# Performance work log

Measured on AMD Instinct MI355X. Metric: run time of the kernel, lower is better.

The kernel has to match this reference:

```python
import jax, jax.numpy as jnp
import numpy as np

NEG_SLOPE = 0.2  # PyG GATConv default negative_slope


def gat_layer(x, src, dst, W, att_src, att_dst, bias, heads, out_ch, n_nodes):
    """PyG-style GATConv (concat=True, add_self_loops already applied via src/dst).
    x: [N, F_in], W: [F_in, heads*out_ch], att_*: [heads, out_ch], bias: [heads*out_ch].
    Returns [N, heads*out_ch]."""
    xh = (x @ W).reshape(n_nodes, heads, out_ch)            # [N,H,C]
    a_src = jnp.einsum('nhc,hc->nh', xh, att_src)           # [N,H]
    a_dst = jnp.einsum('nhc,hc->nh', xh, att_dst)           # [N,H]
    e = a_src[src] + a_dst[dst]                             # [E,H]
    e = jax.nn.leaky_relu(e, NEG_SLOPE)
    # softmax over edges sharing the same destination node
    emax = jax.ops.segment_max(e, dst, num_segments=n_nodes)    # [N,H]
    expe = jnp.exp(e - emax[dst])                           # [E,H]
    denom = jax.ops.segment_sum(expe, dst, num_segments=n_nodes)
    coef = expe / (denom[dst] + 1e-16)                      # [E,H]
    # weighted scatter-aggregate of source features
    msg = xh[src] * coef[:, :, None]                        # [E,H,C]
    out = jax.ops.segment_sum(msg, dst, num_segments=n_nodes)  # [N,H,C]
    return out.reshape(n_nodes, heads * out_ch) + bias


def setup_inputs() -> dict:
    key = jax.random.key(0)
    ks = jax.random.split(key, 10)
    N, E = 50000, 800000
    IN, HID, OUT, H = 4, 60, 96, 8
    x = jax.random.normal(ks[0], (N, IN), dtype=jnp.float32)
    edge_index = jax.random.randint(ks[1], (2, E), 0, N, dtype=jnp.int64)
    s = 0.1
    W1 = jax.random.normal(ks[2], (IN, H * HID), dtype=jnp.float32) * s
    att_src1 = jax.random.normal(ks[3], (H, HID), dtype=jnp.float32) * s
    att_dst1 = jax.random.normal(ks[4], (H, HID), dtype=jnp.float32) * s
    b1 = jnp.zeros((H * HID,), dtype=jnp.float32)
    W2 = jax.random.normal(ks[5], (H * HID, OUT), dtype=jnp.float32) * s
    att_src2 = jax.random.normal(ks[6], (1, OUT), dtype=jnp.float32) * s
    att_dst2 = jax.random.normal(ks[7], (1, OUT), dtype=jnp.float32) * s
    b2 = jnp.zeros((OUT,), dtype=jnp.float32)
    return {"x": x, "edge_index": edge_index,
            "W1": W1, "att_src1": att_src1, "att_dst1": att_dst1, "b1": b1,
            "W2": W2, "att_src2": att_src2, "att_dst2": att_dst2, "b2": b2}


def reference(x, edge_index, W1, att_src1, att_dst1, b1, W2, att_src2, att_dst2, b2):
    N = x.shape[0]
    # add self-loops (PyG GATConv default add_self_loops=True)
    loop = jnp.arange(N, dtype=edge_index.dtype)
    src = jnp.concatenate([edge_index[0], loop])
    dst = jnp.concatenate([edge_index[1], loop])
    # dropout layers are identity in eval mode
    h = gat_layer(x, src, dst, W1, att_src1, att_dst1, b1, heads=8, out_ch=60, n_nodes=N)
    h = jax.nn.elu(h)
    out = gat_layer(h, src, dst, W2, att_src2, att_dst2, b2, heads=1, out_ch=96, n_nodes=N)
    return out
```

## Files before the change

### kernel.cpp

```cpp
#include <hip/hip_runtime.h>
#include <hip/hip_bf16.h>
#include <hip/hip_fp16.h>
#include <cstdint>
#include <cstddef>


typedef _Float16 half8 __attribute__((ext_vector_type(8)));
typedef float floatx4 __attribute__((ext_vector_type(4)));

constexpr int BSH = 7;
constexpr int MAXBUK = 512;

__global__ __launch_bounds__(256) void setup_kernel(
    const float* __restrict__ W1,
    const float* __restrict__ as1, const float* __restrict__ ad1,
    const float* __restrict__ W2,
    const float* __restrict__ as2, const float* __restrict__ ad2,
    const float* __restrict__ x, const int* __restrict__ ei,
    int E, int N,
    float4* __restrict__ w1t, float2* __restrict__ wa2t,
    __half* __restrict__ w2t,
    float* __restrict__ a_s1, float* __restrict__ a_d1,
    int* __restrict__ bcnt,
    int NW2T, int NA1)
{
    __shared__ int   lcnt[MAXBUK];
    __shared__ float wa1s[64];
    int b = blockIdx.x;
    int t = threadIdx.x;
    int A1_0 = 1 + NW2T;
    int H0   = A1_0 + NA1;

    if (b == 0) {
        for (int i = t; i < 480; i += 256) {
            float accs = 0.f, accd = 0.f;
            #pragma unroll 4
            for (int c = 0; c < 96; ++c) {
                float w = W2[i * 96 + c];
                accs += w * as2[c];
                accd += w * ad2[c];
            }
            wa2t[i] = make_float2(accs, accd);
            w1t[i]  = make_float4(W1[i], W1[480 + i], W1[960 + i], W1[1440 + i]);
        }
    } else if (b < A1_0) {
        int idx = (b - 1) * 256 + t;
        if (idx < 96 * 480) {
            int n = idx / 480, k = idx - n * 480;
            w2t[idx] = __float2half(W2[k * 96 + n]);
        }
    } else if (b < H0) {
        if (t < 32) {
            int k = t >> 3, h = t & 7;
            float accs = 0.f, accd = 0.f;
            for (int c = 0; c < 60; ++c) {
                float w = W1[k * 480 + h * 60 + c];
                accs += w * as1[h * 60 + c];
                accd += w * ad1[h * 60 + c];
            }
            wa1s[k * 8 + h]      = accs;
            wa1s[32 + k * 8 + h] = accd;
        }
        __syncthreads();
        int n = (b - A1_0) * 256 + t;
        if (n < N) {
            float4 xv = *(const float4*)(x + (size_t)n * 4);
            #pragma unroll
            for (int h = 0; h < 8; ++h) {
                float as = xv.x * wa1s[h] + xv.y * wa1s[8 + h]
                         + xv.z * wa1s[16 + h] + xv.w * wa1s[24 + h];
                float ad = xv.x * wa1s[32 + h] + xv.y * wa1s[40 + h]
                         + xv.z * wa1s[48 + h] + xv.w * wa1s[56 + h];
                a_s1[n * 8 + h] = as;
                a_d1[n * 8 + h] = ad;
            }
        }
    } else {
        int nbuk = (N + 127) >> BSH;
        for (int i = t; i < nbuk; i += 256) lcnt[i] = 0;
        __syncthreads();
        #pragma unroll
        for (int u = 0; u < 8; ++u) {
            int e = (b - H0) * 2048 + u * 256 + t;
            if (e < E + N) {
                int d = (e < E) ? ei[E + e] : (e - E);
                atomicAdd(&lcnt[d >> BSH], 1);
            }
        }
        __syncthreads();
        for (int i = t; i < nbuk; i += 256)
            if (lcnt[i]) atomicAdd(&bcnt[i], lcnt[i]);
    }
}

__global__ __launch_bounds__(512) void bucket_scan(const int* __restrict__ bcnt, int nbuk,
                                                   int* __restrict__ boff,
                                                   int* __restrict__ bcursor,
                                                   int* __restrict__ row_ptr, int N)
{
    __shared__ int wsum[8];
    int t = threadIdx.x, lane = t & 63, wid = t >> 6;
    int v = (t < nbuk) ? bcnt[t] : 0;
    int x = v;
    #pragma unroll
    for (int off = 1; off < 64; off <<= 1) {
        int y = __shfl_up(x, off, 64);
        if (lane >= off) x += y;
    }
    if (lane == 63) wsum[wid] = x;
    __syncthreads();
    if (wid == 0) {
        int wv = (lane < 8) ? wsum[lane] : 0;
        #pragma unroll
        for (int off = 1; off < 8; off <<= 1) {
            int y = __shfl_up(wv, off, 64);
            if (lane >= off) wv += y;
        }
        if (lane < 8) wsum[lane] = wv;
    }
    __syncthreads();
    int excl = (wid ? wsum[wid - 1] : 0) + x - v;
    if (t < nbuk) { boff[t] = excl; bcursor[t] = excl; }
    if (t == nbuk - 1) { boff[nbuk] = excl + v; row_ptr[N] = excl + v; }
}

__global__ __launch_bounds__(256) void multisplit(const int* __restrict__ ei, int E, int N,
                                                  int* __restrict__ bcursor,
                                                  int2* __restrict__ ebuf)
{
    __shared__ int lcnt[MAXBUK];
    __shared__ int lbase[MAXBUK];
    int t = threadIdx.x;
    int nbuk = (N + 127) >> BSH;
    for (int b = t; b < nbuk; b += 256) lcnt[b] = 0;
    __syncthreads();
    constexpr int U = 16;
    int ss[U], dd[U], rk[U];
    bool ok[U];
    #pragma unroll
    for (int u = 0; u < U; ++u) {
        int e = blockIdx.x * (256 * U) + u * 256 + t;
        ok[u] = e < E + N;
        if (ok[u]) {
            if (e < E) { ss[u] = ei[e]; dd[u] = ei[E + e]; } else { ss[u] = dd[u] = e - E; }
            rk[u] = atomicAdd(&lcnt[dd[u] >> BSH], 1);
        }
    }
    __syncthreads();
    for (int b = t; b < nbuk; b += 256)
        lbase[b] = lcnt[b] ? atomicAdd(&bcursor[b], lcnt[b]) : 0;
    __syncthreads();
    #pragma unroll
    for (int u = 0; u < U; ++u)
        if (ok[u]) ebuf[(size_t)lbase[dd[u] >> BSH] + rk[u]] = make_int2(ss[u], dd[u]);
}

__global__ __launch_bounds__(256) void csrfill2(const int2* __restrict__ ebuf,
                                                const int* __restrict__ boff,
                                                int* __restrict__ row_ptr,
                                                int* __restrict__ csr,
                                                int* __restrict__ csrdst, int N)
{
    int b = blockIdx.x;
    int node0 = b << BSH;
    int nnode = N - node0;  if (nnode > 128) nnode = 128;
    int beg = boff[b], end = boff[b + 1];
    __shared__ int hcnt[128], hcur[128];
    __shared__ int wends[4];
    int t = threadIdx.x;
    if (t < 128) hcnt[t] = 0;
    __syncthreads();
    for (int i = beg + t; i < end; i += 256)
        atomicAdd(&hcnt[ebuf[i].y - node0], 1);
    __syncthreads();
    int lane = t & 63, wid = t >> 6;
    int v = (t < 128) ? hcnt[t] : 0;
    int x = v;
    #pragma unroll
    for (int off = 1; off < 64; off <<= 1) {
        int y = __shfl_up(x, off, 64);
        if (lane >= off) x += y;
    }
    if (lane == 63) wends[wid] = x;
    __syncthreads();
    int excl = x - v + ((wid == 1) ? wends[0] : 0);
    if (t < 128) {
        hcur[t] = excl;
        if (t < nnode) row_ptr[node0 + t] = beg + excl;
    }
    __syncthreads();
    for (int i = beg + t; i < end; i += 256) {
        int2 e = ebuf[i];
        int p = atomicAdd(&hcur[e.y - node0], 1);
        csr[(size_t)beg + p]    = e.x;
        csrdst[(size_t)beg + p] = e.y;
    }
}

__global__ __launch_bounds__(256) void gat1_agg(
    const int* __restrict__ row_ptr, const int* __restrict__ csr,
    const float* __restrict__ x,
    const float* __restrict__ a_s1, const float* __restrict__ a_d1,
    float* __restrict__ agg, float* __restrict__ ssum, int N)
{
    int gid = blockIdx.x * blockDim.x + threadIdx.x;
    int node = gid >> 6;
    if (node >= N) return;
    int lane = threadIdx.x & 63;
    int half = lane >> 5;
    int sl   = lane & 31;
    int h = sl >> 2, c = sl & 3;
    float adh = a_d1[(size_t)node * 8 + h];

    float aggv = 0.f, sv = 0.f;
    int beg = row_ptr[node], end = row_ptr[node + 1];
    constexpr int U = 4;
    for (int base = beg; base < end; base += 2 * U) {
        int   idx[U];
        float msk[U];
        #pragma unroll
        for (int u = 0; u < U; ++u) {
            int t = base + 2 * u + half;
            msk[u] = (t < end) ? 1.f : 0.f;
            idx[u] = csr[t < end ? t : (end - 1)];
        }
        float xv[U], av[U];
        #pragma unroll
        for (int u = 0; u < U; ++u) xv[u] = x[(size_t)idx[u] * 4 + c];
        #pragma unroll
        for (int u = 0; u < U; ++u) av[u] = a_s1[(size_t)idx[u] * 8 + h];
        #pragma unroll
        for (int u = 0; u < U; ++u) {
            float ev = av[u] + adh;
            ev = ev > 0.f ? ev : 0.2f * ev;
            float p = __expf(ev) * msk[u];
            sv   += p;
            aggv += p * xv[u];
        }
    }
    aggv += __shfl_xor(aggv, 32);
    sv   += __shfl_xor(sv, 32);
    if (lane < 32) {
        agg[(size_t)node * 32 + lane] = aggv;
        if (c == 0) ssum[(size_t)node * 8 + h] = sv;
    }
}

__global__ __launch_bounds__(256) void h_kernel(
    const float* __restrict__ agg, const float* __restrict__ ssum,
    const float4* __restrict__ w1t, const float* __restrict__ b1,
    const float2* __restrict__ wa2t,
    __half* __restrict__ h2buf, float* __restrict__ a2s, float* __restrict__ a2d, int N)
{
    __shared__ float4 w1s[480];
    __shared__ float2 wa2s[480];
    __shared__ float  b1s[480];
    int t = threadIdx.x;
    for (int i = t; i < 480; i += 256) {
        w1s[i]  = w1t[i];
        wa2s[i] = wa2t[i];
        b1s[i]  = b1[i];
    }
    __syncthreads();

    int node = blockIdx.x * 4 + (t >> 6);
    if (node >= N) return;
    int lane = t & 63;
    bool act = lane < 60;

    float psrc = 0.f, pdst = 0.f;
    #pragma unroll
    for (int h = 0; h < 8; ++h) {
        float4 ag  = *(const float4*)(agg + (size_t)node * 32 + h * 4);
        float  inv = 1.f / (ssum[(size_t)node * 8 + h] + 1e-16f);
        if (act) {
            int col = h * 60 + lane;
            float4 w  = w1s[col];
            float raw = ag.x * w.x + ag.y * w.y + ag.z * w.z + ag.w * w.w;
            float v   = raw * inv + b1s[col];
            float o   = v > 0.f ? v : (__expf(v) - 1.f);
            h2buf[(size_t)node * 480 + col] = __float2half(o);
            float2 wz = wa2s[col];
            psrc += o * wz.x;
            pdst += o * wz.y;
        }
    }
    #pragma unroll
    for (int off = 32; off; off >>= 1) {
        psrc += __shfl_xor(psrc, off);
        pdst += __shfl_xor(pdst, off);
    }
    if (lane == 0) { a2s[node] = psrc; a2d[node] = pdst; }
}

__global__ __launch_bounds__(256) void p2_kernel(
    const int* __restrict__ csr, const int* __restrict__ csrdst,
    const float* __restrict__ a_s2, const float* __restrict__ a_d2,
    float* __restrict__ pbuf2, int EP)
{
    int i = (blockIdx.x * 256 + threadIdx.x) * 4;
    if (i + 3 < EP) {
        int4 s4 = *(const int4*)(csr + i);
        int4 d4 = *(const int4*)(csrdst + i);
        float e0 = a_s2[s4.x] + a_d2[d4.x];
        float e1 = a_s2[s4.y] + a_d2[d4.y];
        float e2 = a_s2[s4.z] + a_d2[d4.z];
        float e3 = a_s2[s4.w] + a_d2[d4.w];
        float4 o;
        o.x = __expf(fmaxf(e0, 0.2f * e0));
        o.y = __expf(fmaxf(e1, 0.2f * e1));
        o.z = __expf(fmaxf(e2, 0.2f * e2));
        o.w = __expf(fmaxf(e3, 0.2f * e3));
        *(float4*)(pbuf2 + i) = o;
    } else {
        for (int u = 0; u < 4; ++u) {
            int e = i + u;
            if (e < EP) {
                float ev = a_s2[csr[e]] + a_d2[csrdst[e]];
                pbuf2[e] = __expf(fmaxf(ev, 0.2f * ev));
            }
        }
    }
}

__global__ __launch_bounds__(256) void gemm2_mfma(
    const __half* __restrict__ h2, const __half* __restrict__ w2t,
    __half* __restrict__ xh2h, int N)
{
    int wave = threadIdx.x >> 6;
    int lane = threadIdx.x & 63;
    int m0 = blockIdx.x * 64 + wave * 16;
    int ra   = lane & 15;
    int kgrp = lane >> 4;
    int m = m0 + ra;  if (m > N - 1) m = N - 1;

    floatx4 acc[6];
    #pragma unroll
    for (int n = 0; n < 6; ++n) acc[n] = (floatx4){0.f, 0.f, 0.f, 0.f};

    const _Float16* arow = (const _Float16*)(h2 + (size_t)m * 480);
    const _Float16* wt   = (const _Float16*)w2t;
    for (int k0 = 0; k0 < 480; k0 += 32) {
        half8 af = *(const half8*)(arow + k0 + kgrp * 8);
        #pragma unroll
        for (int n = 0; n < 6; ++n) {
            half8 bf = *(const half8*)(wt + (size_t)(n * 16 + ra) * 480 + k0 + kgrp * 8);
            acc[n] = __builtin_amdgcn_mfma_f32_16x16x32_f16(af, bf, acc[n], 0, 0, 0);
        }
    }
    #pragma unroll
    for (int n = 0; n < 6; ++n) {
        int c = n * 16 + ra;
        #pragma unroll
        for (int j = 0; j < 4; ++j) {
            int r = m0 + kgrp * 4 + j;
            if (r < N) xh2h[(size_t)r * 96 + c] = __float2half(acc[n][j]);
        }
    }
}

__global__ __launch_bounds__(256) void gat2_fused(
    const int* __restrict__ row_ptr, const int* __restrict__ csr,
    const float* __restrict__ pbuf2,
    const __half* __restrict__ xh2h, const float* __restrict__ b2,
    float* __restrict__ out, int N)
{
    int gid = blockIdx.x * blockDim.x + threadIdx.x;
    int node = gid >> 6;
    if (node >= N) return;
    int lane = threadIdx.x & 63;
    bool act = lane < 48;
    float s = 0.f, ax = 0.f, ay = 0.f;
    int beg = __builtin_amdgcn_readfirstlane(row_ptr[node]);
    int end = __builtin_amdgcn_readfirstlane(row_ptr[node + 1]);
    constexpr int U = 16;
    for (int e0 = beg; e0 < end; e0 += U) {
        int   srcs[U];
        float pv[U];
        #pragma unroll
        for (int u = 0; u < U; ++u) {
            int t = e0 + u;  if (t > end - 1) t = end - 1;
            srcs[u] = __builtin_amdgcn_readfirstlane(csr[t]);
            float pr = __uint_as_float(
                __builtin_amdgcn_readfirstlane(__float_as_uint(pbuf2[t])));
            pv[u] = (e0 + u < end) ? pr : 0.f;
        }
        __half2 gv[U];
        if (act) {
            #pragma unroll
            for (int u = 0; u < U; ++u)
                gv[u] = ((const __half2*)(xh2h + (size_t)srcs[u] * 96))[lane];
        }
        #pragma unroll
        for (int u = 0; u < U; ++u) {
            s += pv[u];
            if (act) {
                float2 fg = __half22float2(gv[u]);
                ax += pv[u] * fg.x;
                ay += pv[u] * fg.y;
            }
        }
    }
    float inv = 1.f / (s + 1e-16f);
    if (act) {
        out[(size_t)node * 96 + 2 * lane]     = ax * inv + b2[2 * lane];
        out[(size_t)node * 96 + 2 * lane + 1] = ay * inv + b2[2 * lane + 1];
    }
}

extern "C" void kernel_launch(void* const* d_in, const int* in_sizes, int n_in,
                              void* d_out, int out_size, void* d_ws, size_t ws_size,
                              hipStream_t stream)
{
    const float* x   = (const float*)d_in[0];
    const int*   ei  = (const int*)  d_in[1];
    const float* W1  = (const float*)d_in[2];
    const float* as1 = (const float*)d_in[3];
    const float* ad1 = (const float*)d_in[4];
    const float* b1  = (const float*)d_in[5];
    const float* W2  = (const float*)d_in[6];
    const float* as2 = (const float*)d_in[7];
    const float* ad2 = (const float*)d_in[8];
    const float* b2  = (const float*)d_in[9];
    float* out = (float*)d_out;

    int N  = in_sizes[0] / 4;
    int E  = in_sizes[1] / 2;
    int EP = E + N;
    int NBUK  = (N + 127) >> BSH;
    int NW2T  = (96 * 480 + 255) / 256;
    int NA1   = (N + 255) / 256;
    int NBK_H = (EP + 2047) / 2048;
    int NBK_M = (EP + 4095) / 4096;
    int NSETUP = 1 + NW2T + NA1 + NBK_H;

    float* f = (float*)d_ws;
    float* a_s1  = f;  f += (size_t)N * 8;
    float* a_d1  = f;  f += (size_t)N * 8;
    float* agg   = f;  f += (size_t)N * 32;
    float* ssum  = f;  f += (size_t)N * 8;
    float* a_s2  = f;  f += N;
    float* a_d2  = f;  f += N;
    float4* w1t  = (float4*)f;  f += 480 * 4;
    float2* wa2t = (float2*)f;  f += 480 * 2;
    __half* h2buf = (__half*)f;
    __half* hp   = h2buf + (size_t)N * 480;
    __half* xh2h = hp;   hp += (size_t)N * 96;
    __half* w2t  = hp;   hp += 96 * 480;
    int2* ebuf   = (int2*)hp;
    int* ip      = (int*)(ebuf + EP);
    int* row_ptr = ip;  ip += N + 1;
    int* bcnt    = ip;  ip += MAXBUK;
    int* boff    = ip;  ip += MAXBUK + 1;
    int* bcursor = ip;  ip += MAXBUK;
    int* csr     = ip;  ip += EP;
    int* csrdst  = ip;  ip += EP;
    float* pbuf2 = (float*)ip;  ip += EP;

    size_t needed = (size_t)((char*)ip - (char*)d_ws);
    if (needed > ws_size) return;

    hipMemsetAsync(bcnt, 0, MAXBUK * sizeof(int), stream);
    setup_kernel<<<NSETUP, 256, 0, stream>>>(
        W1, as1, ad1, W2, as2, ad2, x, ei, E, N,
        w1t, wa2t, w2t, a_s1, a_d1, bcnt, NW2T, NA1);
    bucket_scan<<<1, 512, 0, stream>>>(bcnt, NBUK, boff, bcursor, row_ptr, N);
    multisplit<<<NBK_M, 256, 0, stream>>>(ei, E, N, bcursor, ebuf);
    csrfill2<<<NBUK, 256, 0, stream>>>(ebuf, boff, row_ptr, csr, csrdst, N);
    gat1_agg<<<(N * 64 + 255) / 256, 256, 0, stream>>>(
        row_ptr, csr, x, a_s1, a_d1, agg, ssum, N);
    h_kernel<<<(N + 3) / 4, 256, 0, stream>>>(
        agg, ssum, w1t, b1, wa2t, h2buf, a_s2, a_d2, N);
    p2_kernel<<<(EP + 1023) / 1024, 256, 0, stream>>>(
        csr, csrdst, a_s2, a_d2, pbuf2, EP);
    gemm2_mfma<<<(N + 63) / 64, 256, 0, stream>>>(h2buf, w2t, xh2h, N);
    gat2_fused<<<(N * 64 + 255) / 256, 256, 0, stream>>>(
        row_ptr, csr, pbuf2, xh2h, b2, out, N);
}
```

Baseline: 191.8 us.

## Fuse layer-1 edge aggregation into CSR fill using shared-memory atomics per bucket

Merges the CSR fill kernel with the layer-1 GAT aggregation. Each bucket block now computes the per-edge attention weights while it scatters edges, and accumulates the softmax denominators and weighted features in shared memory with atomics. This removes one kernel launch and the second pass that re-read csr and gathered x and a_s1 per node. In exchange there are 40 shared-memory float atomics per edge, possible contention on high-degree destinations, and only about 391 blocks doing all the aggregation work, which may limit parallelism.

```diff
diff --git a/kernel.cpp b/kernel.cpp
--- a/kernel.cpp
+++ b/kernel.cpp
@@ -155,95 +155,105 @@
         if (ok[u]) ebuf[(size_t)lbase[dd[u] >> BSH] + rk[u]] = make_int2(ss[u], dd[u]);
 }
 
-__global__ __launch_bounds__(256) void csrfill2(const int2* __restrict__ ebuf,
-                                                const int* __restrict__ boff,
-                                                int* __restrict__ row_ptr,
-                                                int* __restrict__ csr,
-                                                int* __restrict__ csrdst, int N)
+__global__ __launch_bounds__(256) void csrfill_agg(
+    const int2* __restrict__ ebuf, const int* __restrict__ boff,
+    const float* __restrict__ x,
+    const float* __restrict__ a_s1, const float* __restrict__ a_d1,
+    int* __restrict__ row_ptr, int* __restrict__ csr, int* __restrict__ csrdst,
+    float* __restrict__ agg, float* __restrict__ ssum, int N)
 {
     int b = blockIdx.x;
     int node0 = b << BSH;
     int nnode = N - node0;  if (nnode > 128) nnode = 128;
     int beg = boff[b], end = boff[b + 1];
-    __shared__ int hcnt[128], hcur[128];
-    __shared__ int wends[4];
+    __shared__ int   hcnt[128], hcur[128];
+    __shared__ int   wends[4];
+    __shared__ float ad1s[128][8];
+    __shared__ float aggs[128][33];
+    __shared__ float ssums[128][9];
     int t = threadIdx.x;
+
     if (t < 128) hcnt[t] = 0;
-    __syncthreads();
+    for (int i = t; i < 128 * 33; i += 256) (&aggs[0][0])[i] = 0.f;
+    for (int i = t; i < 128 * 9;  i += 256) (&ssums[0][0])[i] = 0.f;
+    for (int i = t; i < nnode * 8; i += 256)
+        ad1s[i >> 3][i & 7] = a_d1[(size_t)node0 * 8 + i];
+    __syncthreads();
+
     for (int i = beg + t; i < end; i += 256)
         atomicAdd(&hcnt[ebuf[i].y - node0], 1);
     __syncthreads();
+
     int lane = t & 63, wid = t >> 6;
     int v = (t < 128) ? hcnt[t] : 0;
-    int x = v;
+    int xs = v;
     #pragma unroll
     for (int off = 1; off < 64; off <<= 1) {
-        int y = __shfl_up(x, off, 64);
-        if (lane >= off) x += y;
-    }
-    if (lane == 63) wends[wid] = x;
-    __syncthreads();
-    int excl = x - v + ((wid == 1) ? wends[0] : 0);
+        int y = __shfl_up(xs, off, 64);
+        if (lane >= off) xs += y;
+    }
+    if (lane == 63) wends[wid] = xs;
+    __syncthreads();
+    int excl = xs - v + ((wid == 1) ? wends[0] : 0);
     if (t < 128) {
         hcur[t] = excl;
         if (t < nnode) row_ptr[node0 + t] = beg + excl;
     }
     __syncthreads();
-    for (int i = beg + t; i < end; i += 256) {
-        int2 e = ebuf[i];
-        int p = atomicAdd(&hcur[e.y - node0], 1);
-        csr[(size_t)beg + p]    = e.x;
-        csrdst[(size_t)beg + p] = e.y;
-    }
-}
-
-__global__ __launch_bounds__(256) void gat1_agg(
-    const int* __restrict__ row_ptr, const int* __restrict__ csr,
-    const float* __restrict__ x,
-    const float* __restrict__ a_s1, const float* __restrict__ a_d1,
-    float* __restrict__ agg, float* __restrict__ ssum, int N)
-{
-    int gid = blockIdx.x * blockDim.x + threadIdx.x;
-    int node = gid >> 6;
-    if (node >= N) return;
-    int lane = threadIdx.x & 63;
-    int half = lane >> 5;
-    int sl   = lane & 31;
-    int h = sl >> 2, c = sl & 3;
-    float adh = a_d1[(size_t)node * 8 + h];
-
-    float aggv = 0.f, sv = 0.f;
-    int beg = row_ptr[node], end = row_ptr[node + 1];
-    constexpr int U = 4;
-    for (int base = beg; base < end; base += 2 * U) {
-        int   idx[U];
-        float msk[U];
-        #pragma unroll
-        for (int u = 0; u < U; ++u) {
-            int t = base + 2 * u + half;
-            msk[u] = (t < end) ? 1.f : 0.f;
-            idx[u] = csr[t < end ? t : (end - 1)];
-        }
-        float xv[U], av[U];
-        #pragma unroll
-        for (int u = 0; u < U; ++u) xv[u] = x[(size_t)idx[u] * 4 + c];
-        #pragma unroll
-        for (int u = 0; u < U; ++u) av[u] = a_s1[(size_t)idx[u] * 8 + h];
-        #pragma unroll
-        for (int u = 0; u < U; ++u) {
-            float ev = av[u] + adh;
-            ev = ev > 0.f ? ev : 0.2f * ev;
-            float p = __expf(ev) * msk[u];
-            sv   += p;
-            aggv += p * xv[u];
-        }
-    }
-    aggv += __shfl_xor(aggv, 32);
-    sv   += __shfl_xor(sv, 32);
-    if (lane < 32) {
-        agg[(size_t)node * 32 + lane] = aggv;
-        if (c == 0) ssum[(size_t)node * 8 + h] = sv;
-    }
+
+    for (int i = beg + t; i < end; i += 512) {
+        int  i1 = i + 256;
+        bool ok1 = i1 < end;
+        int2 e0 = ebuf[i];
+        int2 e1 = ok1 ? ebuf[i1] : e0;
+        float4 xv0 = *(const float4*)(x + (size_t)e0.x * 4);
+        float4 xv1 = *(const float4*)(x + (size_t)e1.x * 4);
+        float4 asa0 = *(const float4*)(a_s1 + (size_t)e0.x * 8);
+        float4 asb0 = *(const float4*)(a_s1 + (size_t)e0.x * 8 + 4);
+        float4 asa1 = *(const float4*)(a_s1 + (size_t)e1.x * 8);
+        float4 asb1 = *(const float4*)(a_s1 + (size_t)e1.x * 8 + 4);
+
+        int dl0 = e0.y - node0;
+        int p0 = atomicAdd(&hcur[dl0], 1);
+        csr[(size_t)beg + p0]    = e0.x;
+        csrdst[(size_t)beg + p0] = e0.y;
+        {
+            float as[8] = {asa0.x, asa0.y, asa0.z, asa0.w, asb0.x, asb0.y, asb0.z, asb0.w};
+            float xv[4] = {xv0.x, xv0.y, xv0.z, xv0.w};
+            #pragma unroll
+            for (int h = 0; h < 8; ++h) {
+                float ev = as[h] + ad1s[dl0][h];
+                float pv = __expf(fmaxf(ev, 0.2f * ev));
+                atomicAdd(&ssums[dl0][h], pv);
+                #pragma unroll
+                for (int c = 0; c < 4; ++c)
+                    atomicAdd(&aggs[dl0][h * 4 + c], pv * xv[c]);
+            }
+        }
+        if (ok1) {
+            int dl1 = e1.y - node0;
+            int p1 = atomicAdd(&hcur[dl1], 1);
+            csr[(size_t)beg + p1]    = e1.x;
+            csrdst[(size_t)beg + p1] = e1.y;
+            float as[8] = {asa1.x, asa1.y, asa1.z, asa1.w, asb1.x, asb1.y, asb1.z, asb1.w};
+            float xv[4] = {xv1.x, xv1.y, xv1.z, xv1.w};
+            #pragma unroll
+            for (int h = 0; h < 8; ++h) {
+                float ev = as[h] + ad1s[dl1][h];
+                float pv = __expf(fmaxf(ev, 0.2f * ev));
+                atomicAdd(&ssums[dl1][h], pv);
+                #pragma unroll
+                for (int c = 0; c < 4; ++c)
+                    atomicAdd(&aggs[dl1][h * 4 + c], pv * xv[c]);
+            }
+        }
+    }
+    __syncthreads();
+
+    for (int i = t; i < nnode * 32; i += 256)
+        agg[(size_t)node0 * 32 + i] = aggs[i >> 5][i & 31];
+    for (int i = t; i < nnode * 8; i += 256)
+        ssum[(size_t)node0 * 8 + i] = ssums[i >> 3][i & 7];
 }
 
 __global__ __launch_bounds__(256) void h_kernel(
@@ -466,9 +476,8 @@
         w1t, wa2t, w2t, a_s1, a_d1, bcnt, NW2T, NA1);
     bucket_scan<<<1, 512, 0, stream>>>(bcnt, NBUK, boff, bcursor, row_ptr, N);
     multisplit<<<NBK_M, 256, 0, stream>>>(ei, E, N, bcursor, ebuf);
-    csrfill2<<<NBUK, 256, 0, stream>>>(ebuf, boff, row_ptr, csr, csrdst, N);
-    gat1_agg<<<(N * 64 + 255) / 256, 256, 0, stream>>>(
-        row_ptr, csr, x, a_s1, a_d1, agg, ssum, N);
+    csrfill_agg<<<NBUK, 256, 0, stream>>>(
+        ebuf, boff, x, a_s1, a_d1, row_ptr, csr, csrdst, agg, ssum, N);
     h_kernel<<<(N + 3) / 4, 256, 0, stream>>>(
         agg, ssum, w1t, b1, wa2t, h2buf, a_s2, a_d2, N);
     p2_kernel<<<(EP + 1023) / 1024, 256, 0, stream>>>(
```

After: 390.3 us. +103.5%, slower.
